# Kernel tuning notes

Hardware: AMD Instinct MI355X
Metric: run time of the kernel (lower is better)

The kernel has to match this reference:

```python
import jax, jax.numpy as jnp
import numpy as np

N = 16000      # points
K = 16         # neighbors per query (fixed-degree CSR)
M = N * K      # attention pairs
C = 384        # embed_dim
H = 6          # num_heads
HD = C // H    # head_dim = 64
L = 25         # quant_grid_length = window/quant = 6.0/0.24
T2 = 2 * L - 1 # rel-pos table length = 49
WIN = 6.0
QUANT = 0.24
SCALE = HD ** -0.5


def setup_inputs() -> dict:
    key = jax.random.key(0)
    ks = jax.random.split(key, 12)
    feats = jax.random.normal(ks[0], (N, C), jnp.float32)
    xyz = jax.random.uniform(ks[1], (N, 3), jnp.float32) * 240.0
    index_0 = jnp.repeat(jnp.arange(N, dtype=jnp.int32), K)            # sorted query ids per pair
    index_0_offsets = jnp.arange(0, M + 1, K, dtype=jnp.int32)         # CSR offsets
    index_1 = jax.random.randint(ks[2], (M,), 0, N, jnp.int32)         # key ids per pair
    sort_idx = jax.random.permutation(ks[3], N).astype(jnp.int32)
    lin = lambda k: jax.random.normal(k, (C, C), jnp.float32) * 0.02
    tab = lambda k: jax.random.normal(k, (T2, 3, H, HD), jnp.float32) * 0.02
    return {
        'feats': feats, 'xyz': xyz,
        'index_0': index_0, 'index_0_offsets': index_0_offsets,
        'index_1': index_1, 'sort_idx': sort_idx,
        'Wq': lin(ks[4]), 'bq': jnp.zeros((C,), jnp.float32),
        'Wk': lin(ks[5]), 'bk': jnp.zeros((C,), jnp.float32),
        'Wv': lin(ks[6]), 'bv': jnp.zeros((C,), jnp.float32),
        'Wp': lin(ks[7]), 'bp': jnp.zeros((C,), jnp.float32),
        'Tq': tab(ks[8]), 'Tk': tab(ks[9]), 'Tv': tab(ks[10]),
    }


def reference(feats, xyz, index_0, index_0_offsets, index_1, sort_idx,
              Wq, bq, Wk, bk, Wv, bv, Wp, bp, Tq, Tk, Tv):
    n = feats.shape[0]
    # QKV projections (key/value default to query feats in the module)
    q = (feats @ Wq.T + bq).reshape(n, H, HD) * SCALE
    k = (feats @ Wk.T + bk).reshape(n, H, HD)
    v = (feats @ Wv.T + bv).reshape(n, H, HD)
    # sort into contiguous-window order
    qs, ks_, vs = q[sort_idx], k[sort_idx], v[sort_idx]
    xyz_s = xyz[sort_idx]
    # quantized in-window coords (shift_win=False -> shift 0)
    xq = jnp.floor(((xyz_s - xyz_s.min(0)) % WIN) / QUANT)             # [N,3], values in [0, L-1]
    i0, i1 = index_0, index_1
    rel_idx = (xq[i0] - xq[i1]).astype(jnp.int32) + (L - 1)            # [M,3] in [0, 2L-2]
    # attention logits: q.k plus contextual relative-position terms
    attn = jnp.einsum('mhd,mhd->mh', qs[i0], ks_[i1])                  # [M,H]
    for t in range(3):
        dq = jnp.einsum('nhd,lhd->nlh', qs, Tq[:, t])                  # [N,T2,H]
        dk = jnp.einsum('nhd,lhd->nlh', ks_, Tk[:, t])
        attn = attn + dq[i0, rel_idx[:, t]] + dk[i1, rel_idx[:, t]]
    # scatter softmax over CSR segments (segments given by index_0)
    amax = jax.ops.segment_max(attn, i0, num_segments=n)
    e = jnp.exp(attn - amax[i0])
    denom = jax.ops.segment_sum(e, i0, num_segments=n)
    a = e / denom[i0]                                                  # [M,H]
    # weighted value aggregation
    x = jax.ops.segment_sum(a[:, :, None] * vs[i1], i0, num_segments=n)  # [N,H,HD]
    # relative-position value contribution, factored through table bins
    for t in range(3):
        seg2 = i0 * T2 + rel_idx[:, t]
        w = jax.ops.segment_sum(a, seg2, num_segments=n * T2).reshape(n, T2, H)
        x = x + jnp.einsum('nlh,lhd->nhd', w, Tv[:, t])
    # unsort back to input order and project
    out = jnp.zeros_like(x).at[sort_idx].set(x).reshape(n, C)
    return out @ Wp.T + bp
```

## Files before the change

kernel.cpp:

```cpp
#include <hip/hip_runtime.h>
#include <hip/hip_bf16.h>
#include <cstdint>
#include <cstddef>

#define NPTS 16000
#define MPAD 16128
#define KNB  16
#define CDIM 384
#define NH   6
#define HDIM 64
#define T2C  49
#define NL3T 147
#define DQPAD 896
#define NXC  2944
#define ROWB 4096

static constexpr float WIN    = 6.0f;
static constexpr float QUANT  = 0.24f;
static constexpr float QSCALE = 0.125f;
static constexpr float DQS    = 8.0f;
static constexpr float DQSINV = 0.125f;

typedef __attribute__((ext_vector_type(8))) short short8;
typedef __attribute__((ext_vector_type(4))) float floatx4;
typedef __attribute__((ext_vector_type(4))) unsigned short ushort4v;

__device__ inline unsigned short f2bf(float x) {
    unsigned int u = __float_as_uint(x);
    unsigned int r = (u + 0x7fffu + ((u >> 16) & 1u)) >> 16;
    return (unsigned short)r;
}
__device__ inline float bf2f(unsigned short b) {
    return __uint_as_float(((unsigned int)b) << 16);
}
__device__ inline float f8tof(unsigned char b) {
    return __builtin_amdgcn_cvt_f32_fp8((int)b, 0);
}

__global__ void init_min_kernel(unsigned int* minbits) {
    if (threadIdx.x < 3) minbits[threadIdx.x] = 0x7f800000u;
}

__global__ void min_kernel(const float* __restrict__ xyz,
                           unsigned int* __restrict__ minbits) {
    float m0 = INFINITY, m1 = INFINITY, m2 = INFINITY;
    for (int i = blockIdx.x * blockDim.x + threadIdx.x; i < NPTS;
         i += gridDim.x * blockDim.x) {
        m0 = fminf(m0, xyz[i * 3 + 0]);
        m1 = fminf(m1, xyz[i * 3 + 1]);
        m2 = fminf(m2, xyz[i * 3 + 2]);
    }
#pragma unroll
    for (int off = 1; off < 64; off <<= 1) {
        m0 = fminf(m0, __shfl_xor(m0, off, 64));
        m1 = fminf(m1, __shfl_xor(m1, off, 64));
        m2 = fminf(m2, __shfl_xor(m2, off, 64));
    }
    if ((threadIdx.x & 63) == 0) {
        atomicMin(&minbits[0], __float_as_uint(m0));
        atomicMin(&minbits[1], __float_as_uint(m1));
        atomicMin(&minbits[2], __float_as_uint(m2));
    }
}

__global__ void xq_kernel(const float* __restrict__ xyz,
                          const int* __restrict__ sort_idx,
                          const unsigned int* __restrict__ minbits,
                          int* __restrict__ xq) {
    int n = blockIdx.x * blockDim.x + threadIdx.x;
    if (n >= NPTS) return;
    int orig = sort_idx[n];
#pragma unroll
    for (int t = 0; t < 3; ++t) {
        float mn = __uint_as_float(minbits[t]);
        float v  = xyz[orig * 3 + t] - mn;
        float md = fmodf(v, WIN);
        float q  = floorf(md / QUANT);
        xq[n * 3 + t] = (int)q;
    }
}

__global__ void relpack_kernel(const int* __restrict__ idx1,
                               const int* __restrict__ xq,
                               unsigned int* __restrict__ pairs) {
    int m = blockIdx.x * blockDim.x + threadIdx.x;
    if (m >= NPTS * KNB) return;
    int n = m >> 4;
    int key = idx1[m];
    int r0 = xq[n * 3 + 0] - xq[key * 3 + 0] + 24; r0 = min(max(r0, 0), T2C - 1);
    int r1 = xq[n * 3 + 1] - xq[key * 3 + 1] + 24; r1 = min(max(r1, 0), T2C - 1);
    int r2 = xq[n * 3 + 2] - xq[key * 3 + 2] + 24; r2 = min(max(r2, 0), T2C - 1);
    pairs[m] = (unsigned)key | ((unsigned)r0 << 14) | ((unsigned)r1 << 20) |
               ((unsigned)r2 << 26);
}

#define G0 (NPTS * CDIM / 4)
#define G1 (3 * CDIM * CDIM)
#define G2 (CDIM * CDIM)
#define G3 (NL3T * NH * HDIM)
#define G4 (3 * CDIM)
#define G5 (CDIM)
__global__ void prep_kernel(const float* __restrict__ feats,
                            const int* __restrict__ sortix,
                            const float* __restrict__ Wq,
                            const float* __restrict__ Wk,
                            const float* __restrict__ Wv,
                            const float* __restrict__ Wp,
                            const float* __restrict__ bq,
                            const float* __restrict__ bk,
                            const float* __restrict__ bv,
                            const float* __restrict__ bp,
                            const float* __restrict__ Tv,
                            unsigned short* __restrict__ featsbf,
                            unsigned short* __restrict__ Wall,
                            unsigned short* __restrict__ Wpbf,
                            unsigned short* __restrict__ Tvbf,
                            float* __restrict__ bfull,
                            float* __restrict__ bproj) {
    int i = blockIdx.x * blockDim.x + threadIdx.x;
    if (i < G0) {
        int n  = i / (CDIM / 4);
        int c4 = (i % (CDIM / 4)) * 4;
        const float4 v = *(const float4*)&feats[(size_t)sortix[n] * CDIM + c4];
        ushort4v o;
        o.x = f2bf(v.x); o.y = f2bf(v.y); o.z = f2bf(v.z); o.w = f2bf(v.w);
        *(ushort4v*)&featsbf[(size_t)n * CDIM + c4] = o;
        return;
    }
    i -= G0;
    if (i < G1) {
        int j = i / CDIM, k = i % CDIM;
        float v = (j < 384) ? Wq[j * CDIM + k]
                : (j < 768) ? Wk[(j - 384) * CDIM + k]
                            : Wv[(j - 768) * CDIM + k];
        Wall[i] = f2bf(v);
        return;
    }
    i -= G1;
    if (i < G2) { Wpbf[i] = f2bf(Wp[i]); return; }
    i -= G2;
    if (i < G3) { Tvbf[i] = f2bf(Tv[i]); return; }
    i -= G3;
    if (i < G4) {
        bfull[i] = (i < 384) ? bq[i] : (i < 768) ? bk[i - 384] : bv[i - 768];
        return;
    }
    i -= G4;
    if (i < G5) { bproj[i] = bp[i]; }
}

__global__ __launch_bounds__(384) void weff_kernel(
    const float* __restrict__ Wq, const float* __restrict__ Wk,
    const float* __restrict__ bq, const float* __restrict__ bk,
    const float* __restrict__ Tq, const float* __restrict__ Tk,
    unsigned short* __restrict__ Wall, float* __restrict__ bfull) {
    const int rr   = blockIdx.x;
    const bool isk = blockIdx.y != 0;
    const int base = isk ? 2048 : 1152;
    const float sc = (isk ? 1.0f : QSCALE) * DQS;
    const float* W = isk ? Wk : Wq;
    const float* bv = isk ? bk : bq;
    const float* T = isk ? Tk : Tq;
    const int c = threadIdx.x;

    if (rr >= NL3T * NH) {
        Wall[(size_t)(base + rr) * CDIM + c] = 0;
        if (c == 0) bfull[base + rr] = 0.0f;
        return;
    }
    const int h = rr % NH;

    __shared__ float Trow[HDIM];
    if (c < HDIM) Trow[c] = T[(size_t)rr * HDIM + c];
    __syncthreads();

    float acc = 0.0f;
#pragma unroll
    for (int d = 0; d < HDIM; ++d)
        acc += Trow[d] * W[(size_t)(h * HDIM + d) * CDIM + c];
    Wall[(size_t)(base + rr) * CDIM + c] = f2bf(acc * sc);

    if (c == 0) {
        float bacc = 0.0f;
#pragma unroll
        for (int d = 0; d < HDIM; ++d) bacc += Trow[d] * bv[h * HDIM + d];
        bfull[base + rr] = bacc * sc;
    }
}

__global__ __launch_bounds__(512) void gemm_big(
    const unsigned short* __restrict__ Abf,
    const unsigned short* __restrict__ Wmat,
    const float* __restrict__ bias,
    int mode,
    unsigned char* __restrict__ QXb, float* __restrict__ outf) {
    __shared__ unsigned short As[256 * 64];
    __shared__ unsigned short Bs[128 * 64];
    const int tid  = threadIdx.x;
    const int lane = tid & 63;
    const int w    = tid >> 6;
    const int wm   = w >> 1, wn = w & 1;

    const int nwg  = gridDim.x * gridDim.y;
    const int orig = blockIdx.y * gridDim.x + blockIdx.x;
    const int qq   = nwg >> 3, rr = nwg & 7;
    const int xcd  = orig & 7, idx = orig >> 3;
    const int wg   = (xcd < rr ? xcd * (qq + 1) : rr * (qq + 1) + (xcd - rr) * qq) + idx;
    const int jn0  = (wg % gridDim.x) * 128;
    const int m0   = (wg / gridDim.x) * 256;

    floatx4 acc[4][4];
#pragma unroll
    for (int i = 0; i < 4; ++i)
#pragma unroll
        for (int j = 0; j < 4; ++j) acc[i][j] = (floatx4)0.0f;

    for (int kt = 0; kt < 6; ++kt) {
        const int k0 = kt * 64;
        const int col = (lane & 7) * 8;
#pragma unroll
        for (int q = 0; q < 4; ++q) {
            const int s   = w * 4 + q;
            const int row = s * 8 + (lane >> 3);
            const unsigned short* ga = Abf + (size_t)(m0 + row) * CDIM + k0 + col;
            __builtin_amdgcn_global_load_lds(
                (const __attribute__((address_space(1))) void*)ga,
                (__attribute__((address_space(3))) void*)&As[s * 512], 16, 0, 0);
        }
#pragma unroll
        for (int q = 0; q < 2; ++q) {
            const int s   = w * 2 + q;
            const int row = s * 8 + (lane >> 3);
            const unsigned short* gb = Wmat + (size_t)(jn0 + row) * CDIM + k0 + col;
            __builtin_amdgcn_global_load_lds(
                (const __attribute__((address_space(1))) void*)gb,
                (__attribute__((address_space(3))) void*)&Bs[s * 512], 16, 0, 0);
        }
        __syncthreads();
#pragma unroll
        for (int ks = 0; ks < 2; ++ks) {
            short8 a[4], b[4];
#pragma unroll
            for (int mi = 0; mi < 4; ++mi) {
                int row = wm * 64 + mi * 16 + (lane & 15);
                a[mi] = *(const short8*)&As[row * 64 + ks * 32 + (lane >> 4) * 8];
            }
#pragma unroll
            for (int ni = 0; ni < 4; ++ni) {
                int jr = wn * 64 + ni * 16 + (lane & 15);
                b[ni] = *(const short8*)&Bs[jr * 64 + ks * 32 + (lane >> 4) * 8];
            }
#pragma unroll
            for (int mi = 0; mi < 4; ++mi)
#pragma unroll
                for (int ni = 0; ni < 4; ++ni)
                    acc[mi][ni] = __builtin_amdgcn_mfma_f32_16x16x32_bf16(
                        b[ni], a[mi], acc[mi][ni], 0, 0, 0);
        }
        __syncthreads();
    }

#pragma unroll
    for (int mi = 0; mi < 4; ++mi) {
        const int n = m0 + wm * 64 + mi * 16 + (lane & 15);
#pragma unroll
        for (int ni = 0; ni < 4; ++ni) {
            const int jjb = jn0 + wn * 64 + ni * 16 + (lane >> 4) * 4;
            const float4 b4 = *(const float4*)&bias[jjb];
            const float v0 = acc[mi][ni][0] + b4.x;
            const float v1 = acc[mi][ni][1] + b4.y;
            const float v2 = acc[mi][ni][2] + b4.z;
            const float v3 = acc[mi][ni][3] + b4.w;
            if (mode == 0) {
                unsigned char* rowb = QXb + (size_t)n * ROWB;
                if (jjb < 1152) {
                    const float scl = (jjb < 384) ? QSCALE : 1.0f;
                    ushort4v o;
                    o.x = f2bf(v0 * scl); o.y = f2bf(v1 * scl);
                    o.z = f2bf(v2 * scl); o.w = f2bf(v3 * scl);
                    *(ushort4v*)(rowb + jjb * 2) = o;
                } else {
                    int u = __builtin_amdgcn_cvt_pk_fp8_f32(v0, v1, 0, false);
                    u = __builtin_amdgcn_cvt_pk_fp8_f32(v2, v3, u, true);
                    *(unsigned int*)(rowb + jjb + 1152) = (unsigned int)u;
                }
            } else {
                if (n < NPTS) {
                    float4 o; o.x = v0; o.y = v1; o.z = v2; o.w = v3;
                    *(float4*)&outf[(size_t)n * CDIM + jjb] = o;
                }
            }
        }
    }
}

__global__ __launch_bounds__(384) void attn_kernel(
    const unsigned char* __restrict__ QXb,
    const unsigned int* __restrict__ pairs,
    const unsigned short* __restrict__ Tvbf,
    const int* __restrict__ sortix,
    unsigned short* __restrict__ xb) {
    const int n    = blockIdx.x;
    const int h    = threadIdx.x >> 6;
    const int lane = threadIdx.x & 63;
    const int pp   = lane >> 4, c = lane & 15;

    const unsigned char* qrow = QXb + (size_t)n * ROWB;
    const ushort4v q4 = *(const ushort4v*)(qrow + h * 128 + c * 8);
    const float qx = bf2f(q4.x), qy = bf2f(q4.y), qz = bf2f(q4.z), qw = bf2f(q4.w);

    unsigned int pv[4];
#pragma unroll
    for (int g = 0; g < 4; ++g) pv[g] = pairs[n * KNB + g * 4 + pp];

    const unsigned char* krow[4];
    int j0g[4], j1g[4], j2g[4];
#pragma unroll
    for (int g = 0; g < 4; ++g) {
        krow[g] = QXb + (size_t)(pv[g] & 0x3FFFu) * ROWB;
        j0g[g]  = (int)((pv[g] >> 14) & 63u) * 18;
        j1g[g]  = (int)((pv[g] >> 20) & 63u) * 18 + 6;
        j2g[g]  = (int)(pv[g] >> 26) * 18 + 12;
    }

    float tab[4];
#pragma unroll
    for (int g = 0; g < 4; ++g) {
        tab[g] = DQSINV *
            (f8tof(qrow[2304 + j0g[g] + h]) + f8tof(qrow[2304 + j1g[g] + h]) +
             f8tof(qrow[2304 + j2g[g] + h]) +
             f8tof(krow[g][3200 + j0g[g] + h]) + f8tof(krow[g][3200 + j1g[g] + h]) +
             f8tof(krow[g][3200 + j2g[g] + h]));
    }

    float lg[4];
#pragma unroll
    for (int g = 0; g < 4; ++g) {
        const ushort4v k4 = *(const ushort4v*)(krow[g] + 768 + h * 128 + c * 8);
        lg[g] = qx * bf2f(k4.x) + qy * bf2f(k4.y) + qz * bf2f(k4.z) + qw * bf2f(k4.w);
    }
#pragma unroll
    for (int m = 1; m <= 8; m <<= 1)
#pragma unroll
        for (int g = 0; g < 4; ++g) lg[g] += __shfl_xor(lg[g], m, 64);
#pragma unroll
    for (int g = 0; g < 4; ++g) lg[g] += tab[g];

    float mx = fmaxf(fmaxf(lg[0], lg[1]), fmaxf(lg[2], lg[3]));
    mx = fmaxf(mx, __shfl_xor(mx, 16, 64));
    mx = fmaxf(mx, __shfl_xor(mx, 32, 64));
    float e[4], s = 0.f;
#pragma unroll
    for (int g = 0; g < 4; ++g) { e[g] = expf(lg[g] - mx); s += e[g]; }
    s += __shfl_xor(s, 16, 64);
    s += __shfl_xor(s, 32, 64);
    const float inv = 1.f / s;

    float xa0 = 0.f, xa1 = 0.f, xa2 = 0.f, xa3 = 0.f;
#pragma unroll
    for (int g = 0; g < 4; ++g) {
        const float wgt = e[g] * inv;
        const ushort4v v4 = *(const ushort4v*)(krow[g] + 1536 + h * 128 + c * 8);
        const ushort4v t0 = *(const ushort4v*)&Tvbf[(size_t)(j0g[g] + h) * HDIM + c * 4];
        const ushort4v t1 = *(const ushort4v*)&Tvbf[(size_t)(j1g[g] + h) * HDIM + c * 4];
        const ushort4v t2 = *(const ushort4v*)&Tvbf[(size_t)(j2g[g] + h) * HDIM + c * 4];
        xa0 += wgt * (bf2f(v4.x) + bf2f(t0.x) + bf2f(t1.x) + bf2f(t2.x));
        xa1 += wgt * (bf2f(v4.y) + bf2f(t0.y) + bf2f(t1.y) + bf2f(t2.y));
        xa2 += wgt * (bf2f(v4.z) + bf2f(t0.z) + bf2f(t1.z) + bf2f(t2.z));
        xa3 += wgt * (bf2f(v4.w) + bf2f(t0.w) + bf2f(t1.w) + bf2f(t2.w));
    }
#pragma unroll
    for (int m = 16; m <= 32; m <<= 1) {
        xa0 += __shfl_xor(xa0, m, 64);
        xa1 += __shfl_xor(xa1, m, 64);
        xa2 += __shfl_xor(xa2, m, 64);
        xa3 += __shfl_xor(xa3, m, 64);
    }
    if (pp == 0) {
        const int dst = sortix[n];
        ushort4v o;
        o.x = f2bf(xa0); o.y = f2bf(xa1); o.z = f2bf(xa2); o.w = f2bf(xa3);
        *(ushort4v*)&xb[(size_t)dst * CDIM + h * HDIM + c * 4] = o;
    }
}

extern "C" void kernel_launch(void* const* d_in, const int* in_sizes, int n_in,
                              void* d_out, int out_size, void* d_ws,
                              size_t ws_size, hipStream_t stream) {
    const float* feats  = (const float*)d_in[0];
    const float* xyz    = (const float*)d_in[1];
    const int*   index1 = (const int*)d_in[4];
    const int*   sortix = (const int*)d_in[5];
    const float* Wq = (const float*)d_in[6];
    const float* bq = (const float*)d_in[7];
    const float* Wk = (const float*)d_in[8];
    const float* bk = (const float*)d_in[9];
    const float* Wv = (const float*)d_in[10];
    const float* bv = (const float*)d_in[11];
    const float* Wp = (const float*)d_in[12];
    const float* bp = (const float*)d_in[13];
    const float* Tq = (const float*)d_in[14];
    const float* Tk = (const float*)d_in[15];
    const float* Tv = (const float*)d_in[16];
    float* out = (float*)d_out;

    char* ws = (char*)d_ws;
    size_t off = 0;
    auto alloc = [&](size_t bytes) -> void* {
        void* p = ws + off;
        off = (off + bytes + 255) & ~(size_t)255;
        return p;
    };
    unsigned short* featsbf = (unsigned short*)alloc((size_t)MPAD * CDIM * 2);
    unsigned short* Wall    = (unsigned short*)alloc((size_t)NXC * CDIM * 2);
    unsigned short* Wpbf    = (unsigned short*)alloc((size_t)CDIM * CDIM * 2);
    unsigned short* Tvbf    = (unsigned short*)alloc((size_t)NL3T * NH * HDIM * 2);
    float*          bfull   = (float*)alloc((size_t)NXC * sizeof(float));
    float*          bproj   = (float*)alloc((size_t)CDIM * sizeof(float));
    unsigned char*  QXb     = (unsigned char*)alloc((size_t)MPAD * ROWB);
    unsigned int*   pairs   = (unsigned int*)alloc((size_t)NPTS * KNB * 4);
    int*            xq      = (int*)alloc((size_t)NPTS * 3 * sizeof(int));
    unsigned int*   minbits = (unsigned int*)alloc(16);
    unsigned short* xb      = featsbf;

    init_min_kernel<<<1, 64, 0, stream>>>(minbits);
    min_kernel<<<128, 256, 0, stream>>>(xyz, minbits);
    xq_kernel<<<(NPTS + 255) / 256, 256, 0, stream>>>(xyz, sortix, minbits, xq);
    relpack_kernel<<<(NPTS * KNB + 255) / 256, 256, 0, stream>>>(index1, xq, pairs);

    const int prep_total = G0 + G1 + G2 + G3 + G4 + G5;
    prep_kernel<<<(prep_total + 255) / 256, 256, 0, stream>>>(
        feats, sortix, Wq, Wk, Wv, Wp, bq, bk, bv, bp, Tv,
        featsbf, Wall, Wpbf, Tvbf, bfull, bproj);

    dim3 gw(DQPAD, 2);
    weff_kernel<<<gw, 384, 0, stream>>>(Wq, Wk, bq, bk, Tq, Tk, Wall, bfull);

    dim3 g0(NXC / 128, MPAD / 256);
    gemm_big<<<g0, 512, 0, stream>>>(featsbf, Wall, bfull, 0, QXb,
                                     (float*)nullptr);

    attn_kernel<<<NPTS, 384, 0, stream>>>(QXb, pairs, Tvbf, sortix, xb);

    dim3 g1(CDIM / 128, MPAD / 256);
    gemm_big<<<g1, 512, 0, stream>>>(xb, Wpbf, bproj, 1, (unsigned char*)nullptr,
                                     out);
}
```

Baseline: 253.8 us.

## Fold key relative-position term into attention dot product and shrink GEMM tiles

The key-side contextual position term is no longer precomputed as extra GEMM output columns. Instead the attention kernel adds the summed bf16 Tk rows to the query before the q·k dot product. This removes 896 GEMM output columns and shrinks the per-row QX buffer, cutting GEMM FLOPs and memory traffic. It adds three small table gathers per neighbour in attention. The GEMM also moves to 128x128 tiles with 256 threads, and the padding of rows from 16000 to 16128 is dropped because 16000 divides evenly by 128.

```diff
diff --git a/kernel.cpp b/kernel.cpp
--- a/kernel.cpp
+++ b/kernel.cpp
@@ -4,7 +4,6 @@
 #include <cstddef>
 
 #define NPTS 16000
-#define MPAD 16128
 #define KNB  16
 #define CDIM 384
 #define NH   6
@@ -12,8 +11,8 @@
 #define T2C  49
 #define NL3T 147
 #define DQPAD 896
-#define NXC  2944
-#define ROWB 4096
+#define NXC  2048
+#define ROWB 3200
 
 static constexpr float WIN    = 6.0f;
 static constexpr float QUANT  = 0.24f;
@@ -98,6 +97,7 @@
 #define G1 (3 * CDIM * CDIM)
 #define G2 (CDIM * CDIM)
 #define G3 (NL3T * NH * HDIM)
+#define G3B (NL3T * NH * HDIM)
 #define G4 (3 * CDIM)
 #define G5 (CDIM)
 __global__ void prep_kernel(const float* __restrict__ feats,
@@ -111,10 +111,12 @@
                             const float* __restrict__ bv,
                             const float* __restrict__ bp,
                             const float* __restrict__ Tv,
+                            const float* __restrict__ Tk,
                             unsigned short* __restrict__ featsbf,
                             unsigned short* __restrict__ Wall,
                             unsigned short* __restrict__ Wpbf,
                             unsigned short* __restrict__ Tvbf,
+                            unsigned short* __restrict__ Tkbf,
                             float* __restrict__ bfull,
                             float* __restrict__ bproj) {
     int i = blockIdx.x * blockDim.x + threadIdx.x;
@@ -141,6 +143,8 @@
     i -= G2;
     if (i < G3) { Tvbf[i] = f2bf(Tv[i]); return; }
     i -= G3;
+    if (i < G3B) { Tkbf[i] = f2bf(Tk[i]); return; }
+    i -= G3B;
     if (i < G4) {
         bfull[i] = (i < 384) ? bq[i] : (i < 768) ? bk[i - 384] : bv[i - 768];
         return;
@@ -150,51 +154,45 @@
 }
 
 __global__ __launch_bounds__(384) void weff_kernel(
-    const float* __restrict__ Wq, const float* __restrict__ Wk,
-    const float* __restrict__ bq, const float* __restrict__ bk,
-    const float* __restrict__ Tq, const float* __restrict__ Tk,
+    const float* __restrict__ Wq, const float* __restrict__ bq,
+    const float* __restrict__ Tq,
     unsigned short* __restrict__ Wall, float* __restrict__ bfull) {
-    const int rr   = blockIdx.x;
-    const bool isk = blockIdx.y != 0;
-    const int base = isk ? 2048 : 1152;
-    const float sc = (isk ? 1.0f : QSCALE) * DQS;
-    const float* W = isk ? Wk : Wq;
-    const float* bv = isk ? bk : bq;
-    const float* T = isk ? Tk : Tq;
-    const int c = threadIdx.x;
+    const int rr = blockIdx.x;
+    const int c  = threadIdx.x;
+    const float sc = QSCALE * DQS;
 
     if (rr >= NL3T * NH) {
-        Wall[(size_t)(base + rr) * CDIM + c] = 0;
-        if (c == 0) bfull[base + rr] = 0.0f;
+        Wall[(size_t)(1152 + rr) * CDIM + c] = 0;
+        if (c == 0) bfull[1152 + rr] = 0.0f;
         return;
     }
     const int h = rr % NH;
 
     __shared__ float Trow[HDIM];
-    if (c < HDIM) Trow[c] = T[(size_t)rr * HDIM + c];
+    if (c < HDIM) Trow[c] = Tq[(size_t)rr * HDIM + c];
     __syncthreads();
 
     float acc = 0.0f;
 #pragma unroll
     for (int d = 0; d < HDIM; ++d)
-        acc += Trow[d] * W[(size_t)(h * HDIM + d) * CDIM + c];
-    Wall[(size_t)(base + rr) * CDIM + c] = f2bf(acc * sc);
+        acc += Trow[d] * Wq[(size_t)(h * HDIM + d) * CDIM + c];
+    Wall[(size_t)(1152 + rr) * CDIM + c] = f2bf(acc * sc);
 
     if (c == 0) {
         float bacc = 0.0f;
 #pragma unroll
-        for (int d = 0; d < HDIM; ++d) bacc += Trow[d] * bv[h * HDIM + d];
-        bfull[base + rr] = bacc * sc;
-    }
-}
-
-__global__ __launch_bounds__(512) void gemm_big(
+        for (int d = 0; d < HDIM; ++d) bacc += Trow[d] * bq[h * HDIM + d];
+        bfull[1152 + rr] = bacc * sc;
+    }
+}
+
+__global__ __launch_bounds__(256) void gemm_big(
     const unsigned short* __restrict__ Abf,
     const unsigned short* __restrict__ Wmat,
     const float* __restrict__ bias,
     int mode,
     unsigned char* __restrict__ QXb, float* __restrict__ outf) {
-    __shared__ unsigned short As[256 * 64];
+    __shared__ unsigned short As[128 * 64];
     __shared__ unsigned short Bs[128 * 64];
     const int tid  = threadIdx.x;
     const int lane = tid & 63;
@@ -207,7 +205,7 @@
     const int xcd  = orig & 7, idx = orig >> 3;
     const int wg   = (xcd < rr ? xcd * (qq + 1) : rr * (qq + 1) + (xcd - rr) * qq) + idx;
     const int jn0  = (wg % gridDim.x) * 128;
-    const int m0   = (wg / gridDim.x) * 256;
+    const int m0   = (wg / gridDim.x) * 128;
 
     floatx4 acc[4][4];
 #pragma unroll
@@ -217,21 +215,16 @@
 
     for (int kt = 0; kt < 6; ++kt) {
         const int k0 = kt * 64;
-        const int col = (lane & 7) * 8;
 #pragma unroll
         for (int q = 0; q < 4; ++q) {
-            const int s   = w * 4 + q;
-            const int row = s * 8 + (lane >> 3);
-            const unsigned short* ga = Abf + (size_t)(m0 + row) * CDIM + k0 + col;
+            const int s    = w * 4 + q;
+            const int row  = s * 8 + (lane >> 3);
+            const int col  = (lane & 7) * 8;
+            const unsigned short* ga = Abf  + (size_t)(m0  + row) * CDIM + k0 + col;
+            const unsigned short* gb = Wmat + (size_t)(jn0 + row) * CDIM + k0 + col;
             __builtin_amdgcn_global_load_lds(
                 (const __attribute__((address_space(1))) void*)ga,
                 (__attribute__((address_space(3))) void*)&As[s * 512], 16, 0, 0);
-        }
-#pragma unroll
-        for (int q = 0; q < 2; ++q) {
-            const int s   = w * 2 + q;
-            const int row = s * 8 + (lane >> 3);
-            const unsigned short* gb = Wmat + (size_t)(jn0 + row) * CDIM + k0 + col;
             __builtin_amdgcn_global_load_lds(
                 (const __attribute__((address_space(1))) void*)gb,
                 (__attribute__((address_space(3))) void*)&Bs[s * 512], 16, 0, 0);
@@ -285,10 +278,8 @@
                     *(unsigned int*)(rowb + jjb + 1152) = (unsigned int)u;
                 }
             } else {
-                if (n < NPTS) {
-                    float4 o; o.x = v0; o.y = v1; o.z = v2; o.w = v3;
-                    *(float4*)&outf[(size_t)n * CDIM + jjb] = o;
-                }
+                float4 o; o.x = v0; o.y = v1; o.z = v2; o.w = v3;
+                *(float4*)&outf[(size_t)n * CDIM + jjb] = o;
             }
         }
     }
@@ -297,6 +288,7 @@
 __global__ __launch_bounds__(384) void attn_kernel(
     const unsigned char* __restrict__ QXb,
     const unsigned int* __restrict__ pairs,
+    const unsigned short* __restrict__ Tkbf,
     const unsigned short* __restrict__ Tvbf,
     const int* __restrict__ sortix,
     unsigned short* __restrict__ xb) {
@@ -328,16 +320,22 @@
     for (int g = 0; g < 4; ++g) {
         tab[g] = DQSINV *
             (f8tof(qrow[2304 + j0g[g] + h]) + f8tof(qrow[2304 + j1g[g] + h]) +
-             f8tof(qrow[2304 + j2g[g] + h]) +
-             f8tof(krow[g][3200 + j0g[g] + h]) + f8tof(krow[g][3200 + j1g[g] + h]) +
-             f8tof(krow[g][3200 + j2g[g] + h]));
+             f8tof(qrow[2304 + j2g[g] + h]));
     }
 
     float lg[4];
 #pragma unroll
     for (int g = 0; g < 4; ++g) {
         const ushort4v k4 = *(const ushort4v*)(krow[g] + 768 + h * 128 + c * 8);
-        lg[g] = qx * bf2f(k4.x) + qy * bf2f(k4.y) + qz * bf2f(k4.z) + qw * bf2f(k4.w);
+        const ushort4v t0 = *(const ushort4v*)&Tkbf[(size_t)(j0g[g] + h) * HDIM + c * 4];
+        const ushort4v t1 = *(const ushort4v*)&Tkbf[(size_t)(j1g[g] + h) * HDIM + c * 4];
+        const ushort4v t2 = *(const ushort4v*)&Tkbf[(size_t)(j2g[g] + h) * HDIM + c * 4];
+        const float tk0 = bf2f(t0.x) + bf2f(t1.x) + bf2f(t2.x);
+        const float tk1 = bf2f(t0.y) + bf2f(t1.y) + bf2f(t2.y);
+        const float tk2 = bf2f(t0.z) + bf2f(t1.z) + bf2f(t2.z);
+        const float tk3 = bf2f(t0.w) + bf2f(t1.w) + bf2f(t2.w);
+        lg[g] = bf2f(k4.x) * (qx + tk0) + bf2f(k4.y) * (qy + tk1) +
+                bf2f(k4.z) * (qz + tk2) + bf2f(k4.w) * (qw + tk3);
     }
 #pragma unroll
     for (int m = 1; m <= 8; m <<= 1)
@@ -411,13 +409,14 @@
         off = (off + bytes + 255) & ~(size_t)255;
         return p;
     };
-    unsigned short* featsbf = (unsigned short*)alloc((size_t)MPAD * CDIM * 2);
+    unsigned short* featsbf = (unsigned short*)alloc((size_t)NPTS * CDIM * 2);
     unsigned short* Wall    = (unsigned short*)alloc((size_t)NXC * CDIM * 2);
     unsigned short* Wpbf    = (unsigned short*)alloc((size_t)CDIM * CDIM * 2);
     unsigned short* Tvbf    = (unsigned short*)alloc((size_t)NL3T * NH * HDIM * 2);
+    unsigned short* Tkbf    = (unsigned short*)alloc((size_t)NL3T * NH * HDIM * 2);
     float*          bfull   = (float*)alloc((size_t)NXC * sizeof(float));
     float*          bproj   = (float*)alloc((size_t)CDIM * sizeof(float));
-    unsigned char*  QXb     = (unsigned char*)alloc((size_t)MPAD * ROWB);
+    unsigned char*  QXb     = (unsigned char*)alloc((size_t)NPTS * ROWB);
     unsigned int*   pairs   = (unsigned int*)alloc((size_t)NPTS * KNB * 4);
     int*            xq      = (int*)alloc((size_t)NPTS * 3 * sizeof(int));
     unsigned int*   minbits = (unsigned int*)alloc(16);
@@ -428,21 +427,20 @@
     xq_kernel<<<(NPTS + 255) / 256, 256, 0, stream>>>(xyz, sortix, minbits, xq);
     relpack_kernel<<<(NPTS * KNB + 255) / 256, 256, 0, stream>>>(index1, xq, pairs);
 
-    const int prep_total = G0 + G1 + G2 + G3 + G4 + G5;
+    const int prep_total = G0 + G1 + G2 + G3 + G3B + G4 + G5;
     prep_kernel<<<(prep_total + 255) / 256, 256, 0, stream>>>(
-        feats, sortix, Wq, Wk, Wv, Wp, bq, bk, bv, bp, Tv,
-        featsbf, Wall, Wpbf, Tvbf, bfull, bproj);
-
-    dim3 gw(DQPAD, 2);
-    weff_kernel<<<gw, 384, 0, stream>>>(Wq, Wk, bq, bk, Tq, Tk, Wall, bfull);
-
-    dim3 g0(NXC / 128, MPAD / 256);
-    gemm_big<<<g0, 512, 0, stream>>>(featsbf, Wall, bfull, 0, QXb,
+        feats, sortix, Wq, Wk, Wv, Wp, bq, bk, bv, bp, Tv, Tk,
+        featsbf, Wall, Wpbf, Tvbf, Tkbf, bfull, bproj);
+
+    weff_kernel<<<DQPAD, 384, 0, stream>>>(Wq, bq, Tq, Wall, bfull);
+
+    dim3 g0(NXC / 128, NPTS / 128);
+    gemm_big<<<g0, 256, 0, stream>>>(featsbf, Wall, bfull, 0, QXb,
                                      (float*)nullptr);
 
-    attn_kernel<<<NPTS, 384, 0, stream>>>(QXb, pairs, Tvbf, sortix, xb);
-
-    dim3 g1(CDIM / 128, MPAD / 256);
-    gemm_big<<<g1, 512, 0, stream>>>(xb, Wpbf, bproj, 1, (unsigned char*)nullptr,
+    attn_kernel<<<NPTS, 384, 0, stream>>>(QXb, pairs, Tkbf, Tvbf, sortix, xb);
+
+    dim3 g1(CDIM / 128, NPTS / 128);
+    gemm_big<<<g1, 256, 0, stream>>>(xb, Wpbf, bproj, 1, (unsigned char*)nullptr,
                                      out);
 }
```

New measurement: 262.2 us. 3.3% more time.
